# Optimization experiments

Hardware: AMD Instinct MI355X
Metric: run time of the kernel (lower is better)

Reference implementation:

```python
import jax, jax.numpy as jnp
import numpy as np
from jax import lax

M = 512      # num_centers
K = 32       # neighbors per center
FEAT = 256   # token feature dim
EPS = 1e-5   # BatchNorm eps


def fps(xyz, m):
    """Furthest point sampling. xyz: (B,N,3) -> idx (B,m) int32."""
    B, N, _ = xyz.shape
    first = jnp.zeros((B,), jnp.int32)

    def step(carry, _):
        min_d, last = carry                       # (B,N), (B,)
        last_pt = jnp.take_along_axis(xyz, last[:, None, None], axis=1)  # (B,1,3)
        d = jnp.sum((xyz - last_pt) ** 2, axis=-1)                       # (B,N)
        min_d = jnp.minimum(min_d, d)
        nxt = jnp.argmax(min_d, axis=1).astype(jnp.int32)
        return (min_d, nxt), nxt

    init = (jnp.full((B, N), 1e10, jnp.float32), first)
    _, rest = lax.scan(step, init, None, length=m - 1)   # (m-1, B)
    return jnp.concatenate([first[None, :], rest], axis=0).T  # (B,m)


def bn(x, g, b, mean, var):
    return (x - mean) * (g * lax.rsqrt(var + EPS)) + b


def setup_inputs() -> dict:
    key = jax.random.key(0)
    ks = jax.random.split(key, 16)
    B, N = 8, 16384
    r = lambda k_, s, sc=0.1: jax.random.normal(k_, s, jnp.float32) * sc
    inp = {
        "xyz": jax.random.normal(ks[0], (B, N, 3), jnp.float32),
        "W1": r(ks[1], (64, 3)), "b1": r(ks[2], (64,)),
        "g1": 1.0 + r(ks[3], (64,)), "be1": r(ks[4], (64,)),
        "m1": r(ks[5], (64,)), "v1": 1.0 + 0.1 * jax.random.uniform(ks[6], (64,)),
        "W2": r(ks[7], (128, 64)), "b2": r(ks[8], (128,)),
        "g2": 1.0 + r(ks[9], (128,)), "be2": r(ks[10], (128,)),
        "m2": r(ks[11], (128,)), "v2": 1.0 + 0.1 * jax.random.uniform(ks[12], (128,)),
        "W3": r(ks[13], (FEAT, 128)), "b3": r(ks[14], (FEAT,)),
        "Wp": r(ks[15], (FEAT, 3)), "bp": jnp.zeros((FEAT,), jnp.float32),
    }
    return inp


def reference(xyz, W1, b1, g1, be1, m1, v1, W2, b2, g2, be2, m2, v2, W3, b3, Wp, bp):
    B, N, _ = xyz.shape
    # --- FPS centers ---
    idx_c = fps(xyz, M)                                            # (B,M)
    centers = jnp.take_along_axis(xyz, idx_c[:, :, None], axis=1)  # (B,M,3)
    # --- brute-force KNN ---
    dist = jnp.sum((centers[:, :, None, :] - xyz[:, None, :, :]) ** 2, axis=-1)  # (B,M,N)
    _, idx = lax.top_k(-dist, K)                                   # (B,M,K)
    nbrs = jnp.take_along_axis(
        xyz, idx.reshape(B, M * K)[:, :, None], axis=1
    ).reshape(B, M, K, 3)
    grouped = nbrs - centers[:, :, None, :]                        # (B,M,K,3)
    # --- MiniPointNet: 1x1 convs == channel matmuls, eval-mode BN ---
    h = jnp.einsum("bmkc,oc->bmko", grouped, W1) + b1
    h = jax.nn.relu(bn(h, g1, be1, m1, v1))
    h = jnp.einsum("bmkc,oc->bmko", h, W2) + b2
    h = jax.nn.relu(bn(h, g2, be2, m2, v2))
    h = jnp.einsum("bmkc,oc->bmko", h, W3) + b3
    tokens = jnp.max(h, axis=2)                                    # (B,M,FEAT)
    pos = jnp.einsum("bmc,oc->bmo", centers, Wp) + bp
    return centers, tokens + pos
```

## Files before the change

### kernel.cpp

```cpp
#include <hip/hip_runtime.h>

typedef unsigned int u32;
typedef unsigned long long u64;
typedef unsigned short u16;

#define DEVFN static __device__ __forceinline__

constexpr int NPTS = 16384;
constexpr int NC = 512;

typedef __attribute__((ext_vector_type(8))) short bf16x8;
typedef __attribute__((ext_vector_type(4))) float f32x4;

#define MFMA16(a, b, c) __builtin_amdgcn_mfma_f32_16x16x32_bf16(a, b, c, 0, 0, 0)

DEVFN u16 bf16rne(float f) {
  u32 b = __float_as_uint(f);
  u32 r = (b + 0x7FFFu + ((b >> 16) & 1u)) >> 16;
  return (u16)r;
}

DEVFN u64 shflx64(u64 v, int m) {
  u32 lo = __shfl_xor((u32)v, m, 64);
  u32 hi = __shfl_xor((u32)(v >> 32), m, 64);
  return ((u64)hi << 32) | lo;
}
DEVFN u64 shfl64(u64 v, int src) {
  u32 lo = __shfl((u32)v, src, 64);
  u32 hi = __shfl((u32)(v >> 32), src, 64);
  return ((u64)hi << 32) | lo;
}

DEVFN void csw(u64& a, u64& b) {
  u64 lo = a < b ? a : b;
  u64 hi = a < b ? b : a;
  a = lo; b = hi;
}

DEVFN u32 spread3(u32 v) {
  return (v & 1u) | ((v & 2u) << 2) | ((v & 4u) << 4) | ((v & 8u) << 6);
}

DEVFN u64 maxf64u(u64 a, u64 b) {
  double x = __longlong_as_double((long long)a);
  double y = __longlong_as_double((long long)b);
  return (u64)__double_as_longlong(fmax(x, y));
}
template <int CTRL, int RM>
DEVFN u64 dppmaxf(u64 k) {
  u32 lo = (u32)k, hi = (u32)(k >> 32);
  u32 lo2 = (u32)__builtin_amdgcn_update_dpp((int)lo, (int)lo, CTRL, RM, 0xF, false);
  u32 hi2 = (u32)__builtin_amdgcn_update_dpp((int)hi, (int)hi, CTRL, RM, 0xF, false);
  return maxf64u(k, ((u64)hi2 << 32) | lo2);
}
DEVFN u64 wavemaxf(u64 k) {
  k = dppmaxf<0x121, 0xF>(k);
  k = dppmaxf<0x122, 0xF>(k);
  k = dppmaxf<0x124, 0xF>(k);
  k = dppmaxf<0x128, 0xF>(k);
  k = dppmaxf<0x142, 0xA>(k);
  k = dppmaxf<0x143, 0xC>(k);
  return k;
}

__global__ __launch_bounds__(1024) void fps_kernel(const float* __restrict__ xyz,
                                                   float* __restrict__ centers,
                                                   float4* __restrict__ ws4) {
  const int b = blockIdx.x;
  const int t = threadIdx.x;
  const int lane = t & 63;
  const int w = t >> 6;
  const float* xb = xyz + (size_t)b * NPTS * 3;
  const int bo = b * NPTS;

  __shared__ char smem[78336];
  float* mdL = (float*)smem;
  u64* ckeyL = (u64*)(smem + 65536);
  float* bboxT = (float*)(smem + 67584);
  float* ccoordL = (float*)(smem + 73728);
  u16* wl = (u16*)(smem + 76800);
  u32* wcnt = (u32*)(smem + 77824);
  float* redB = (float*)(smem + 77832);
  u32* redW = (u32*)(smem + 78248);
  u32* hist = (u32*)smem;
  u16* soidx = (u16*)(smem + 8192);

  const u32 inf10 = __float_as_uint(1e10f);

  u32 mcode[16];
  {
    float ox[16], oy[16], oz[16];
    float lx = 1e30f, ly = 1e30f, lz = 1e30f;
    float hx = -1e30f, hy = -1e30f, hz = -1e30f;
#pragma unroll
    for (int j = 0; j < 16; ++j) {
      int p = t + j * 1024;
      ox[j] = xb[p * 3 + 0];
      oy[j] = xb[p * 3 + 1];
      oz[j] = xb[p * 3 + 2];
      lx = fminf(lx, ox[j]); hx = fmaxf(hx, ox[j]);
      ly = fminf(ly, oy[j]); hy = fmaxf(hy, oy[j]);
      lz = fminf(lz, oz[j]); hz = fmaxf(hz, oz[j]);
    }
#pragma unroll
    for (int s = 32; s; s >>= 1) {
      lx = fminf(lx, __shfl_xor(lx, s, 64)); hx = fmaxf(hx, __shfl_xor(hx, s, 64));
      ly = fminf(ly, __shfl_xor(ly, s, 64)); hy = fmaxf(hy, __shfl_xor(hy, s, 64));
      lz = fminf(lz, __shfl_xor(lz, s, 64)); hz = fmaxf(hz, __shfl_xor(hz, s, 64));
    }
    if (lane == 0) {
      redB[w * 6 + 0] = lx; redB[w * 6 + 1] = hx;
      redB[w * 6 + 2] = ly; redB[w * 6 + 3] = hy;
      redB[w * 6 + 4] = lz; redB[w * 6 + 5] = hz;
    }
    hist[t] = 0; hist[t + 1024] = 0;
    if (t < 2) wcnt[t] = 0;
    __syncthreads();
    if (t == 0) {
      float a0 = redB[0], a1 = redB[1], a2 = redB[2], a3 = redB[3], a4 = redB[4], a5 = redB[5];
      for (int q = 1; q < 16; ++q) {
        a0 = fminf(a0, redB[q * 6 + 0]); a1 = fmaxf(a1, redB[q * 6 + 1]);
        a2 = fminf(a2, redB[q * 6 + 2]); a3 = fmaxf(a3, redB[q * 6 + 3]);
        a4 = fminf(a4, redB[q * 6 + 4]); a5 = fmaxf(a5, redB[q * 6 + 5]);
      }
      redB[96] = a0; redB[97] = a1; redB[98] = a2;
      redB[99] = a3; redB[100] = a4; redB[101] = a5;
    }
    __syncthreads();
    const float glx = redB[96], ghx = redB[97];
    const float gly = redB[98], ghy = redB[99];
    const float glz = redB[100], ghz = redB[101];
    const float sx = 15.999f / fmaxf(ghx - glx, 1e-9f);
    const float sy = 15.999f / fmaxf(ghy - gly, 1e-9f);
    const float sz = 7.999f / fmaxf(ghz - glz, 1e-9f);
#pragma unroll
    for (int j = 0; j < 16; ++j) {
      int ix = min(15, max(0, (int)((ox[j] - glx) * sx)));
      int iy = min(15, max(0, (int)((oy[j] - gly) * sy)));
      int iz = min(7, max(0, (int)((oz[j] - glz) * sz)));
      mcode[j] = spread3((u32)ix) | (spread3((u32)iy) << 1) | (spread3((u32)iz) << 2);
    }
  }
#pragma unroll
  for (int j = 0; j < 16; ++j) atomicAdd(&hist[mcode[j]], 1u);
  __syncthreads();
  {
    u32 h0 = hist[t * 2 + 0], h1 = hist[t * 2 + 1];
    u32 s = h0 + h1;
    u32 incl = s;
#pragma unroll
    for (int d = 1; d < 64; d <<= 1) {
      u32 n = __shfl_up(incl, d, 64);
      if (lane >= d) incl += n;
    }
    if (lane == 63) redW[w] = incl;
    __syncthreads();
    if (t == 0) {
      u32 run = 0;
      for (int q = 0; q < 16; ++q) { u32 tmp = redW[q]; redW[q] = run; run += tmp; }
    }
    __syncthreads();
    u32 exc = incl - s + redW[w];
    hist[t * 2 + 0] = exc;
    hist[t * 2 + 1] = exc + h0;
    __syncthreads();
  }
#pragma unroll
  for (int j = 0; j < 16; ++j) {
    u32 p = (u32)(t + j * 1024);
    u32 pos = atomicAdd(&hist[mcode[j]], 1u);
    soidx[pos] = (u16)p;
  }
  __syncthreads();
  {
    const int c = t >> 2;
    const int q = t & 3;
    float bxl = 1e30f, bxh = -1e30f, byl = 1e30f, byh = -1e30f, bzl = 1e30f, bzh = -1e30f;
    u32 lomax = 0;
    float axc = 0.f, ayc = 0.f, azc = 0.f;
#pragma unroll
    for (int j = 0; j < 16; ++j) {
      int sp = c * 64 + q * 16 + j;
      u32 oidx = (u32)soidx[sp];
      float X = xb[oidx * 3 + 0];
      float Y = xb[oidx * 3 + 1];
      float Z = xb[oidx * 3 + 2];
      u32 lo = ((16383u - oidx) << 8) | (u32)c;
      float4 pk; pk.x = X; pk.y = Y; pk.z = Z; pk.w = __uint_as_float(lo);
      ws4[bo + sp] = pk;
      if (lo > lomax) { lomax = lo; axc = X; ayc = Y; azc = Z; }
      bxl = fminf(bxl, X); bxh = fmaxf(bxh, X);
      byl = fminf(byl, Y); byh = fmaxf(byh, Y);
      bzl = fminf(bzl, Z); bzh = fmaxf(bzh, Z);
    }
    u32 gl = lomax;
#pragma unroll
    for (int s = 1; s <= 2; s <<= 1) {
      bxl = fminf(bxl, __shfl_xor(bxl, s, 64)); bxh = fmaxf(bxh, __shfl_xor(bxh, s, 64));
      byl = fminf(byl, __shfl_xor(byl, s, 64)); byh = fmaxf(byh, __shfl_xor(byh, s, 64));
      bzl = fminf(bzl, __shfl_xor(bzl, s, 64)); bzh = fmaxf(bzh, __shfl_xor(bzh, s, 64));
      gl = max(gl, (u32)__shfl_xor(gl, s, 64));
    }
    if (lomax == gl) {
      ccoordL[c * 3 + 0] = axc; ccoordL[c * 3 + 1] = ayc; ccoordL[c * 3 + 2] = azc;
    }
    if (q == 0) {
      bboxT[0 * 256 + c] = bxl; bboxT[1 * 256 + c] = bxh;
      bboxT[2 * 256 + c] = byl; bboxT[3 * 256 + c] = byh;
      bboxT[4 * 256 + c] = bzl; bboxT[5 * 256 + c] = bzh;
      ckeyL[c] = ((u64)inf10 << 32) | gl;
    }
  }
  __syncthreads();
#pragma unroll
  for (int j = 0; j < 16; ++j) mdL[t + j * 1024] = 1e10f;

  float cx = xb[0], cy = xb[1], cz = xb[2];
  if (t == 0) {
    centers[(b * NC) * 3 + 0] = cx;
    centers[(b * NC) * 3 + 1] = cy;
    centers[(b * NC) * 3 + 2] = cz;
  }

  for (int i = 1; i < NC; ++i) {
    if (t < 256) {
      float mdm = __uint_as_float((u32)(ckeyL[t] >> 32));
      float ax = fmaxf(0.f, fmaxf(__fsub_rn(bboxT[0 * 256 + t], cx), __fsub_rn(cx, bboxT[1 * 256 + t])));
      float ay = fmaxf(0.f, fmaxf(__fsub_rn(bboxT[2 * 256 + t], cy), __fsub_rn(cy, bboxT[3 * 256 + t])));
      float az = fmaxf(0.f, fmaxf(__fsub_rn(bboxT[4 * 256 + t], cz), __fsub_rn(cz, bboxT[5 * 256 + t])));
      float dlb = __fadd_rn(__fadd_rn(__fmul_rn(ax, ax), __fmul_rn(ay, ay)), __fmul_rn(az, az));
      if (dlb < mdm) {
        u32 pos = atomicAdd(&wcnt[i & 1], 1u);
        wl[(i & 1) * 256 + pos] = (u16)t;
      }
    } else if (t == 512) {
      wcnt[(i + 1) & 1] = 0u;
    }
    __syncthreads();
    {
      const int A = (int)wcnt[i & 1];
      for (int e = w; e < A; e += 16) {
        const int c = (int)wl[(i & 1) * 256 + e];
        const int sp = c * 64 + lane;
        float4 p = ws4[bo + sp];
        float dx = __fsub_rn(p.x, cx);
        float dy = __fsub_rn(p.y, cy);
        float dz = __fsub_rn(p.z, cz);
        float d = __fadd_rn(__fadd_rn(__fmul_rn(dx, dx), __fmul_rn(dy, dy)), __fmul_rn(dz, dz));
        float nm = fminf(mdL[sp], d);
        mdL[sp] = nm;
        u64 key = ((u64)__float_as_uint(nm) << 32) | (u64)__float_as_uint(p.w);
        u64 r = wavemaxf(key);
        u32 klo = (u32)__builtin_amdgcn_readlane((int)(u32)r, 63);
        u32 khi = (u32)__builtin_amdgcn_readlane((int)(u32)(r >> 32), 63);
        u64 wmax = ((u64)khi << 32) | klo;
        if (key == wmax) {
          ckeyL[c] = key;
          ccoordL[c * 3 + 0] = p.x; ccoordL[c * 3 + 1] = p.y; ccoordL[c * 3 + 2] = p.z;
        }
      }
    }
    __syncthreads();
    {
      u64 g0 = ckeyL[lane];
      u64 g1 = ckeyL[lane + 64];
      u64 g2 = ckeyL[lane + 128];
      u64 g3 = ckeyL[lane + 192];
      u64 g = maxf64u(maxf64u(g0, g1), maxf64u(g2, g3));
      g = wavemaxf(g);
      u32 glo = (u32)__builtin_amdgcn_readlane((int)(u32)g, 63);
      u32 widx = glo & 255u;
      cx = ccoordL[widx * 3 + 0];
      cy = ccoordL[widx * 3 + 1];
      cz = ccoordL[widx * 3 + 2];
      if (t == 0) {
        centers[(b * NC + i) * 3 + 0] = cx;
        centers[(b * NC + i) * 3 + 1] = cy;
        centers[(b * NC + i) * 3 + 2] = cz;
      }
    }
  }
}

__global__ __launch_bounds__(512) void knn_kernel(const float* __restrict__ xyz,
                                                  const float* __restrict__ centers,
                                                  float* __restrict__ grouped) {
  __shared__ float spts[1024 * 3];
  __shared__ u64 cand[8][192];
  __shared__ int ccnt[8];
  const int t = threadIdx.x;
  const int lane = t & 63;
  const int w = t >> 6;
  const int cg = blockIdx.x * 8 + w;
  const int b = cg >> 9;
  const float* xb = xyz + (size_t)b * NPTS * 3;
  const float cx = centers[cg * 3 + 0];
  const float cy = centers[cg * 3 + 1];
  const float cz = centers[cg * 3 + 2];
  if (lane == 0) ccnt[w] = 0;

  u64 lmin = ~0ull;
  for (int ch = 0; ch < 16; ++ch) {
    __syncthreads();
    const float* src = xb + ch * 1024 * 3;
#pragma unroll
    for (int q = 0; q < 6; ++q) spts[q * 512 + t] = src[q * 512 + t];
    __syncthreads();
#pragma unroll
    for (int j = 0; j < 16; ++j) {
      int p = lane + j * 64;
      float dx = __fsub_rn(cx, spts[p * 3 + 0]);
      float dy = __fsub_rn(cy, spts[p * 3 + 1]);
      float dz = __fsub_rn(cz, spts[p * 3 + 2]);
      float d = __fadd_rn(__fadd_rn(__fmul_rn(dx, dx), __fmul_rn(dy, dy)), __fmul_rn(dz, dz));
      u64 kk = ((u64)__float_as_uint(d) << 32) | (u64)(u32)(ch * 1024 + p);
      lmin = kk < lmin ? kk : lmin;
    }
  }
  u64 v = lmin;
  for (int k = 2; k <= 64; k <<= 1)
    for (int j = k >> 1; j > 0; j >>= 1) {
      u64 o = shflx64(v, j);
      bool up = ((lane & k) == 0);
      bool lowr = ((lane & j) == 0);
      u64 mn = v < o ? v : o;
      u64 mx = v < o ? o : v;
      v = (lowr == up) ? mn : mx;
    }
  u64 tau = shfl64(v, 31);
  float tf = __uint_as_float((u32)(tau >> 32));

  for (int ch = 0; ch < 16; ++ch) {
    __syncthreads();
    const float* src = xb + ch * 1024 * 3;
#pragma unroll
    for (int q = 0; q < 6; ++q) spts[q * 512 + t] = src[q * 512 + t];
    __syncthreads();
#pragma unroll
    for (int j = 0; j < 16; ++j) {
      int p = lane + j * 64;
      float dx = __fsub_rn(cx, spts[p * 3 + 0]);
      float dy = __fsub_rn(cy, spts[p * 3 + 1]);
      float dz = __fsub_rn(cz, spts[p * 3 + 2]);
      float d = __fadd_rn(__fadd_rn(__fmul_rn(dx, dx), __fmul_rn(dy, dy)), __fmul_rn(dz, dz));
      if (d <= tf) {
        int pos = atomicAdd(&ccnt[w], 1);
        if (pos < 192) cand[w][pos] = ((u64)__float_as_uint(d) << 32) | (u64)(u32)(ch * 1024 + p);
      }
    }
  }
  __syncthreads();
  int cnt = ccnt[w];
  u32 myn = 0u;
  if (cnt <= 192) {
    u64 c0 = (lane < cnt) ? cand[w][lane] : ~0ull;
    u64 c1 = (64 + lane < cnt) ? cand[w][64 + lane] : ~0ull;
    u64 c2 = (128 + lane < cnt) ? cand[w][128 + lane] : ~0ull;
    csw(c0, c1); csw(c1, c2); csw(c0, c1);
    for (int r = 0; r < 32; ++r) {
      u64 wm = c0;
      for (int s = 32; s; s >>= 1) {
        u64 o = shflx64(wm, s);
        wm = o < wm ? o : wm;
      }
      if (c0 == wm) { c0 = c1; c1 = c2; c2 = ~0ull; }
      if (lane == r) myn = (u32)wm;
    }
  } else {
    u64 last = 0ull;
    for (int r = 0; r < 32; ++r) {
      u64 bb = ~0ull;
      for (int j = 0; j < 256; ++j) {
        int p = lane + j * 64;
        float dx = __fsub_rn(cx, xb[p * 3 + 0]);
        float dy = __fsub_rn(cy, xb[p * 3 + 1]);
        float dz = __fsub_rn(cz, xb[p * 3 + 2]);
        float d = __fadd_rn(__fadd_rn(__fmul_rn(dx, dx), __fmul_rn(dy, dy)), __fmul_rn(dz, dz));
        u64 kk = ((u64)__float_as_uint(d) << 32) | (u64)(u32)p;
        if (r == 0 || kk > last)
          if (kk < bb) bb = kk;
      }
      for (int s = 32; s; s >>= 1) {
        u64 o = shflx64(bb, s);
        bb = o < bb ? o : bb;
      }
      last = bb;
      if (lane == r) myn = (u32)bb;
    }
  }
  if (lane < 32) {
    const float nx = xb[(size_t)myn * 3 + 0];
    const float ny = xb[(size_t)myn * 3 + 1];
    const float nz = xb[(size_t)myn * 3 + 2];
    float* gp = grouped + ((size_t)cg * 32 + lane) * 3;
    gp[0] = __fsub_rn(nx, cx);
    gp[1] = __fsub_rn(ny, cy);
    gp[2] = __fsub_rn(nz, cz);
  }
}

__global__ __launch_bounds__(256) void prep_kernel(
    const float* __restrict__ W1, const float* __restrict__ b1,
    const float* __restrict__ g1, const float* __restrict__ be1,
    const float* __restrict__ m1, const float* __restrict__ v1,
    const float* __restrict__ W2, const float* __restrict__ b2,
    const float* __restrict__ g2, const float* __restrict__ be2,
    const float* __restrict__ m2, const float* __restrict__ v2,
    const float* __restrict__ W3,
    float* __restrict__ w1eff, u16* __restrict__ w2L,
    float* __restrict__ t2, u16* __restrict__ w3L) {
  const int tid = blockIdx.x * 256 + threadIdx.x;
  if (tid < 64) {
    float s = g1[tid] / sqrtf(v1[tid] + 1e-5f);
    w1eff[tid * 4 + 0] = W1[tid * 3 + 0] * s;
    w1eff[tid * 4 + 1] = W1[tid * 3 + 1] * s;
    w1eff[tid * 4 + 2] = W1[tid * 3 + 2] * s;
    w1eff[tid * 4 + 3] = (b1[tid] - m1[tid]) * s + be1[tid];
  }
  if (tid < 128) {
    float s = g2[tid] / sqrtf(v2[tid] + 1e-5f);
    t2[tid] = (b2[tid] - m2[tid]) * s + be2[tid];
  }
  if (tid < 8192) {
    int i = tid & 63, o = tid >> 6;
    float s = g2[o] / sqrtf(v2[o] + 1e-5f);
    int kg = i >> 3, j = i & 7;
    w2L[((((kg * 128) + o) * 8) ^ ((kg & 7) * 8)) + j] = bf16rne(W2[o * 64 + i] * s);
  }
  if (tid < 32768) {
    int i = tid & 127, o = tid >> 7;
    int kg = i >> 3, j = i & 7;
    int h = o >> 7, colh = o & 127;
    w3L[h * 16384 + ((((kg * 128) + colh) * 8) ^ ((kg & 7) * 8)) + j] = bf16rne(W3[o * 128 + i]);
  }
}

__global__ __launch_bounds__(256) void mlp_kernel(
    const float* __restrict__ grouped, const u16* __restrict__ w2L,
    const u16* __restrict__ w3L, const float* __restrict__ w1eff,
    const float* __restrict__ t2, const float* __restrict__ b3,
    const float* __restrict__ Wp, const float* __restrict__ bp,
    const float* __restrict__ centers, float* __restrict__ tokens) {
  __shared__ char lds[65536];
  const int t = threadIdx.x;
  const int lane = t & 63;
  const int w = t >> 6;
  const int l15 = lane & 15;
  const int lg = lane >> 4;
  const int c0 = blockIdx.x * 4;
  {
    const u32* s = (const u32*)w2L;
    u32* d = (u32*)lds;
#pragma unroll
    for (int q = 0; q < 16; ++q) d[q * 256 + t] = s[q * 256 + t];
  }
  {
    const int row = t & 127;
    const int oh = (t >> 7) * 32;
    const int cg = c0 + (row >> 5);
    const float* gp = grouped + ((size_t)cg * 32 + (row & 31)) * 3;
    const float gx = gp[0], gy = gp[1], gz = gp[2];
    u16 hv[32];
#pragma unroll
    for (int o = 0; o < 32; ++o) {
      const float4 wvv = ((const float4*)w1eff)[oh + o];
      float h = fmaxf(0.f, gx * wvv.x + gy * wvv.y + gz * wvv.z + wvv.w);
      hv[o] = bf16rne(h);
    }
#pragma unroll
    for (int c4 = 0; c4 < 4; ++c4) {
      uint4 pk;
      pk.x = (u32)hv[c4 * 8 + 0] | ((u32)hv[c4 * 8 + 1] << 16);
      pk.y = (u32)hv[c4 * 8 + 2] | ((u32)hv[c4 * 8 + 3] << 16);
      pk.z = (u32)hv[c4 * 8 + 4] | ((u32)hv[c4 * 8 + 5] << 16);
      pk.w = (u32)hv[c4 * 8 + 6] | ((u32)hv[c4 * 8 + 7] << 16);
      int byte = row * 128 + oh * 2 + c4 * 16;
      *reinterpret_cast<uint4*>(lds + 16384 + (byte ^ ((row & 7) << 4))) = pk;
    }
  }
  __syncthreads();
  f32x4 acc2[2][8];
#pragma unroll
  for (int m = 0; m < 2; ++m)
#pragma unroll
    for (int n = 0; n < 8; ++n) acc2[m][n] = (f32x4){0.f, 0.f, 0.f, 0.f};
#pragma unroll
  for (int ks = 0; ks < 2; ++ks) {
    bf16x8 a[2];
#pragma unroll
    for (int m = 0; m < 2; ++m) {
      int row = w * 32 + m * 16 + l15;
      int byte = row * 128 + (ks * 32 + lg * 8) * 2;
      a[m] = *reinterpret_cast<const bf16x8*>(lds + 16384 + (byte ^ ((row & 7) << 4)));
    }
    const int kg = ks * 4 + lg;
#pragma unroll
    for (int n = 0; n < 8; ++n) {
      int idx = (((kg * 128) + (n * 16 + l15)) * 8) ^ ((kg & 7) * 8);
      bf16x8 bb = *reinterpret_cast<const bf16x8*>((const u16*)lds + idx);
      acc2[0][n] = MFMA16(a[0], bb, acc2[0][n]);
      acc2[1][n] = MFMA16(a[1], bb, acc2[1][n]);
    }
  }
#pragma unroll
  for (int n = 0; n < 8; ++n) {
    const int col = n * 16 + l15;
    const float t2v = t2[col];
#pragma unroll
    for (int m = 0; m < 2; ++m)
#pragma unroll
      for (int r = 0; r < 4; ++r) {
        float vv = fmaxf(0.f, acc2[m][n][r] + t2v);
        int row = w * 32 + m * 16 + lg * 4 + r;
        int byte = row * 256 + col * 2;
        *reinterpret_cast<u16*>(lds + 32768 + (byte ^ ((row & 7) << 4))) = bf16rne(vv);
      }
  }
  __syncthreads();
  const float ccx = centers[(c0 + w) * 3 + 0];
  const float ccy = centers[(c0 + w) * 3 + 1];
  const float ccz = centers[(c0 + w) * 3 + 2];
  float* tok = tokens + (size_t)(c0 + w) * 256;
  for (int h = 0; h < 2; ++h) {
    {
      const u32* s = (const u32*)w3L + h * 8192;
      u32* d = (u32*)lds;
#pragma unroll
      for (int q = 0; q < 32; ++q) d[q * 256 + t] = s[q * 256 + t];
    }
    __syncthreads();
    f32x4 acc3[2][8];
#pragma unroll
    for (int m = 0; m < 2; ++m)
#pragma unroll
      for (int n = 0; n < 8; ++n) acc3[m][n] = (f32x4){0.f, 0.f, 0.f, 0.f};
#pragma unroll
    for (int ks = 0; ks < 4; ++ks) {
      bf16x8 a[2];
#pragma unroll
      for (int m = 0; m < 2; ++m) {
        int row = w * 32 + m * 16 + l15;
        int byte = row * 256 + (ks * 32 + lg * 8) * 2;
        a[m] = *reinterpret_cast<const bf16x8*>(lds + 32768 + (byte ^ ((row & 7) << 4)));
      }
      const int kg = ks * 4 + lg;
#pragma unroll
      for (int n = 0; n < 8; ++n) {
        int idx = (((kg * 128) + (n * 16 + l15)) * 8) ^ ((kg & 7) * 8);
        bf16x8 bb = *reinterpret_cast<const bf16x8*>((const u16*)lds + idx);
        acc3[0][n] = MFMA16(a[0], bb, acc3[0][n]);
        acc3[1][n] = MFMA16(a[1], bb, acc3[1][n]);
      }
    }
#pragma unroll
    for (int n = 0; n < 8; ++n) {
      float vmx = acc3[0][n][0];
#pragma unroll
      for (int m = 0; m < 2; ++m)
#pragma unroll
        for (int r = 0; r < 4; ++r) vmx = fmaxf(vmx, acc3[m][n][r]);
      vmx = fmaxf(vmx, __shfl_xor(vmx, 16, 64));
      vmx = fmaxf(vmx, __shfl_xor(vmx, 32, 64));
      const int col = h * 128 + n * 16 + l15;
      if (lane < 16) {
        float pos = Wp[col * 3 + 0] * ccx + Wp[col * 3 + 1] * ccy +
                    Wp[col * 3 + 2] * ccz + bp[col] + b3[col];
        tok[col] = vmx + pos;
      }
    }
    __syncthreads();
  }
}

extern "C" void kernel_launch(void* const* d_in, const int* in_sizes, int n_in,
                              void* d_out, int out_size, void* d_ws, size_t ws_size,
                              hipStream_t stream) {
  const float* xyz = (const float*)d_in[0];
  const float* W1 = (const float*)d_in[1];
  const float* b1 = (const float*)d_in[2];
  const float* g1 = (const float*)d_in[3];
  const float* be1 = (const float*)d_in[4];
  const float* m1 = (const float*)d_in[5];
  const float* v1 = (const float*)d_in[6];
  const float* W2 = (const float*)d_in[7];
  const float* b2 = (const float*)d_in[8];
  const float* g2 = (const float*)d_in[9];
  const float* be2 = (const float*)d_in[10];
  const float* m2 = (const float*)d_in[11];
  const float* v2 = (const float*)d_in[12];
  const float* W3 = (const float*)d_in[13];
  const float* b3 = (const float*)d_in[14];
  const float* Wp = (const float*)d_in[15];
  const float* bp = (const float*)d_in[16];

  char* ws = (char*)d_ws;
  float4* ws4 = (float4*)ws;
  float* grouped = (float*)ws;
  float* w1eff = (float*)(ws + 2097152);
  u16* w2L = (u16*)(ws + 2098176);
  float* t2 = (float*)(ws + 2114560);
  u16* w3L = (u16*)(ws + 2115072);

  float* centers = (float*)d_out;
  float* tokens = (float*)d_out + 8 * 512 * 3;

  prep_kernel<<<dim3(128), dim3(256), 0, stream>>>(W1, b1, g1, be1, m1, v1,
                                                   W2, b2, g2, be2, m2, v2, W3,
                                                   w1eff, w2L, t2, w3L);
  fps_kernel<<<dim3(8), dim3(1024), 0, stream>>>(xyz, centers, ws4);
  knn_kernel<<<dim3(512), dim3(512), 0, stream>>>(xyz, centers, grouped);
  mlp_kernel<<<dim3(1024), dim3(256), 0, stream>>>(grouped, w2L, w3L, w1eff, t2,
                                                   b3, Wp, bp, centers, tokens);
}
```

Baseline: 832.6 us.

## Move FPS argmax into bbox-test waves and broadcast center via LDS

The per-iteration global argmax over cell keys used to run on all 16 waves. It now runs only in the four waves that do the bounding-box culling, at the start of the next iteration, and the winner is broadcast to the other waves through a small LDS slot. The worklist append switches from one LDS atomic per active thread to one atomic per wave, using a ballot and mbcnt. The wave-max match compares only the low 32 bits, saving one readlane. The goal is less redundant work and fewer atomics on the serial FPS critical path, at the cost of an extra LDS read per iteration and a final argmax after the loop.

```diff
diff --git a/kernel.cpp b/kernel.cpp
--- a/kernel.cpp
+++ b/kernel.cpp
@@ -73,7 +73,7 @@
   const float* xb = xyz + (size_t)b * NPTS * 3;
   const int bo = b * NPTS;
 
-  __shared__ char smem[78336];
+  __shared__ char smem[78352];
   float* mdL = (float*)smem;
   u64* ckeyL = (u64*)(smem + 65536);
   float* bboxT = (float*)(smem + 67584);
@@ -82,6 +82,7 @@
   u32* wcnt = (u32*)(smem + 77824);
   float* redB = (float*)(smem + 77832);
   u32* redW = (u32*)(smem + 78248);
+  float* cxyzL = (float*)(smem + 78336);
   u32* hist = (u32*)smem;
   u16* soidx = (u16*)(smem + 8192);
 
@@ -220,27 +221,54 @@
     centers[(b * NC) * 3 + 0] = cx;
     centers[(b * NC) * 3 + 1] = cy;
     centers[(b * NC) * 3 + 2] = cz;
+    cxyzL[0] = cx; cxyzL[1] = cy; cxyzL[2] = cz;
   }
 
   for (int i = 1; i < NC; ++i) {
     if (t < 256) {
+      if (i > 1) {
+        u64 g0 = ckeyL[lane];
+        u64 g1 = ckeyL[lane + 64];
+        u64 g2 = ckeyL[lane + 128];
+        u64 g3 = ckeyL[lane + 192];
+        u64 g = maxf64u(maxf64u(g0, g1), maxf64u(g2, g3));
+        g = wavemaxf(g);
+        u32 glo = (u32)__builtin_amdgcn_readlane((int)(u32)g, 63);
+        u32 widx = glo & 255u;
+        cx = ccoordL[widx * 3 + 0];
+        cy = ccoordL[widx * 3 + 1];
+        cz = ccoordL[widx * 3 + 2];
+        if (t == 0) {
+          centers[(b * NC + i - 1) * 3 + 0] = cx;
+          centers[(b * NC + i - 1) * 3 + 1] = cy;
+          centers[(b * NC + i - 1) * 3 + 2] = cz;
+          cxyzL[0] = cx; cxyzL[1] = cy; cxyzL[2] = cz;
+        }
+      }
       float mdm = __uint_as_float((u32)(ckeyL[t] >> 32));
       float ax = fmaxf(0.f, fmaxf(__fsub_rn(bboxT[0 * 256 + t], cx), __fsub_rn(cx, bboxT[1 * 256 + t])));
       float ay = fmaxf(0.f, fmaxf(__fsub_rn(bboxT[2 * 256 + t], cy), __fsub_rn(cy, bboxT[3 * 256 + t])));
       float az = fmaxf(0.f, fmaxf(__fsub_rn(bboxT[4 * 256 + t], cz), __fsub_rn(cz, bboxT[5 * 256 + t])));
       float dlb = __fadd_rn(__fadd_rn(__fmul_rn(ax, ax), __fmul_rn(ay, ay)), __fmul_rn(az, az));
-      if (dlb < mdm) {
-        u32 pos = atomicAdd(&wcnt[i & 1], 1u);
-        wl[(i & 1) * 256 + pos] = (u16)t;
-      }
-    } else if (t == 512) {
+      bool act = dlb < mdm;
+      u64 bal = __ballot(act);
+      u32 cnt = (u32)__popcll(bal);
+      u32 base = 0;
+      if (lane == 0) base = atomicAdd(&wcnt[i & 1], cnt);
+      base = (u32)__builtin_amdgcn_readlane((int)base, 0);
+      u32 below = __builtin_amdgcn_mbcnt_hi((u32)(bal >> 32),
+                  __builtin_amdgcn_mbcnt_lo((u32)bal, 0));
+      if (act) wl[(i & 1) * 256 + base + below] = (u16)t;
+    } else if (t == 256) {
       wcnt[(i + 1) & 1] = 0u;
     }
     __syncthreads();
     {
+      cx = cxyzL[0]; cy = cxyzL[1]; cz = cxyzL[2];
       const int A = (int)wcnt[i & 1];
+      const u16* wlp = wl + (i & 1) * 256;
       for (int e = w; e < A; e += 16) {
-        const int c = (int)wl[(i & 1) * 256 + e];
+        const int c = (int)wlp[e];
         const int sp = c * 64 + lane;
         float4 p = ws4[bo + sp];
         float dx = __fsub_rn(p.x, cx);
@@ -251,33 +279,28 @@
         mdL[sp] = nm;
         u64 key = ((u64)__float_as_uint(nm) << 32) | (u64)__float_as_uint(p.w);
         u64 r = wavemaxf(key);
-        u32 klo = (u32)__builtin_amdgcn_readlane((int)(u32)r, 63);
-        u32 khi = (u32)__builtin_amdgcn_readlane((int)(u32)(r >> 32), 63);
-        u64 wmax = ((u64)khi << 32) | klo;
-        if (key == wmax) {
+        u32 rlo = (u32)__builtin_amdgcn_readlane((int)(u32)r, 63);
+        if ((u32)key == rlo) {
           ckeyL[c] = key;
           ccoordL[c * 3 + 0] = p.x; ccoordL[c * 3 + 1] = p.y; ccoordL[c * 3 + 2] = p.z;
         }
       }
     }
     __syncthreads();
-    {
-      u64 g0 = ckeyL[lane];
-      u64 g1 = ckeyL[lane + 64];
-      u64 g2 = ckeyL[lane + 128];
-      u64 g3 = ckeyL[lane + 192];
-      u64 g = maxf64u(maxf64u(g0, g1), maxf64u(g2, g3));
-      g = wavemaxf(g);
-      u32 glo = (u32)__builtin_amdgcn_readlane((int)(u32)g, 63);
-      u32 widx = glo & 255u;
-      cx = ccoordL[widx * 3 + 0];
-      cy = ccoordL[widx * 3 + 1];
-      cz = ccoordL[widx * 3 + 2];
-      if (t == 0) {
-        centers[(b * NC + i) * 3 + 0] = cx;
-        centers[(b * NC + i) * 3 + 1] = cy;
-        centers[(b * NC + i) * 3 + 2] = cz;
-      }
+  }
+  if (w == 0) {
+    u64 g0 = ckeyL[lane];
+    u64 g1 = ckeyL[lane + 64];
+    u64 g2 = ckeyL[lane + 128];
+    u64 g3 = ckeyL[lane + 192];
+    u64 g = maxf64u(maxf64u(g0, g1), maxf64u(g2, g3));
+    g = wavemaxf(g);
+    u32 glo = (u32)__builtin_amdgcn_readlane((int)(u32)g, 63);
+    u32 widx = glo & 255u;
+    if (t == 0) {
+      centers[(b * NC + NC - 1) * 3 + 0] = ccoordL[widx * 3 + 0];
+      centers[(b * NC + NC - 1) * 3 + 1] = ccoordL[widx * 3 + 1];
+      centers[(b * NC + NC - 1) * 3 + 2] = ccoordL[widx * 3 + 2];
     }
   }
 }
```

New measurement: 827.1 us. Within noise of the previous version (-0.7%).

## Restructure FPS loop: static cell-to-wave ownership, one barrier per iteration

Applied to the files above, without the earlier changes.

Each wave now statically owns 16 of the 256 spatial cells and keeps their bounding boxes and best keys in registers. The shared atomic worklist is replaced by a ballot mask over the wave's cells. Each wave publishes its local best key and coordinates into a double-buffered shared slot, and every wave reduces the 16 slots at the start of the next iteration. This removes two of the three block barriers per FPS step and the atomics. The cost is possible load imbalance when active cells cluster on a few waves, plus redundant per-wave reductions.

```diff
diff --git a/kernel.cpp b/kernel.cpp
--- a/kernel.cpp
+++ b/kernel.cpp
@@ -73,15 +73,14 @@
   const float* xb = xyz + (size_t)b * NPTS * 3;
   const int bo = b * NPTS;
 
-  __shared__ char smem[78336];
+  __shared__ char smem[78080];
   float* mdL = (float*)smem;
-  u64* ckeyL = (u64*)(smem + 65536);
-  float* bboxT = (float*)(smem + 67584);
-  float* ccoordL = (float*)(smem + 73728);
-  u16* wl = (u16*)(smem + 76800);
-  u32* wcnt = (u32*)(smem + 77824);
-  float* redB = (float*)(smem + 77832);
-  u32* redW = (u32*)(smem + 78248);
+  float* ccoordL = (float*)(smem + 65536);
+  u32* swb = (u32*)(smem + 68608);
+  u64* ckeyL = (u64*)(smem + 69376);
+  float* bboxT = (float*)(smem + 71424);
+  float* redB = (float*)(smem + 77568);
+  u32* redW = (u32*)(smem + 77984);
   u32* hist = (u32*)smem;
   u16* soidx = (u16*)(smem + 8192);
 
@@ -114,7 +113,6 @@
       redB[w * 6 + 4] = lz; redB[w * 6 + 5] = hz;
     }
     hist[t] = 0; hist[t + 1024] = 0;
-    if (t < 2) wcnt[t] = 0;
     __syncthreads();
     if (t == 0) {
       float a0 = redB[0], a1 = redB[1], a2 = redB[2], a3 = redB[3], a4 = redB[4], a5 = redB[5];
@@ -214,70 +212,118 @@
   __syncthreads();
 #pragma unroll
   for (int j = 0; j < 16; ++j) mdL[t + j * 1024] = 1e10f;
-
-  float cx = xb[0], cy = xb[1], cz = xb[2];
+  u64 ckeyR = 0ull;
+  float rbxl = 0.f, rbxh = 0.f, rbyl = 0.f, rbyh = 0.f, rbzl = 0.f, rbzh = 0.f;
+  if (lane < 16) {
+    const int c = (lane << 4) | w;
+    ckeyR = ckeyL[c];
+    rbxl = bboxT[0 * 256 + c]; rbxh = bboxT[1 * 256 + c];
+    rbyl = bboxT[2 * 256 + c]; rbyh = bboxT[3 * 256 + c];
+    rbzl = bboxT[4 * 256 + c]; rbzh = bboxT[5 * 256 + c];
+  }
+  {
+    u64 v = (lane < 16) ? ckeyR : 0ull;
+    v = wavemaxf(v);
+    u32 vlo = (u32)__builtin_amdgcn_readlane((int)(u32)v, 63);
+    u32 vhi = (u32)__builtin_amdgcn_readlane((int)(u32)(v >> 32), 63);
+    if (lane == 0) {
+      u32 sc = vlo & 255u;
+      u32* dst = swb + 0 * 96 + w * 6;
+      dst[0] = vhi; dst[1] = vlo;
+      dst[2] = __float_as_uint(ccoordL[sc * 3 + 0]);
+      dst[3] = __float_as_uint(ccoordL[sc * 3 + 1]);
+      dst[4] = __float_as_uint(ccoordL[sc * 3 + 2]);
+    }
+  }
   if (t == 0) {
-    centers[(b * NC) * 3 + 0] = cx;
-    centers[(b * NC) * 3 + 1] = cy;
-    centers[(b * NC) * 3 + 2] = cz;
-  }
+    centers[(b * NC) * 3 + 0] = xb[0];
+    centers[(b * NC) * 3 + 1] = xb[1];
+    centers[(b * NC) * 3 + 2] = xb[2];
+  }
+  __syncthreads();
 
   for (int i = 1; i < NC; ++i) {
-    if (t < 256) {
-      float mdm = __uint_as_float((u32)(ckeyL[t] >> 32));
-      float ax = fmaxf(0.f, fmaxf(__fsub_rn(bboxT[0 * 256 + t], cx), __fsub_rn(cx, bboxT[1 * 256 + t])));
-      float ay = fmaxf(0.f, fmaxf(__fsub_rn(bboxT[2 * 256 + t], cy), __fsub_rn(cy, bboxT[3 * 256 + t])));
-      float az = fmaxf(0.f, fmaxf(__fsub_rn(bboxT[4 * 256 + t], cz), __fsub_rn(cz, bboxT[5 * 256 + t])));
+    const u32* sw = swb + ((i - 1) & 1) * 96;
+    const int row = lane & 15;
+    u32 khi = sw[row * 6 + 0];
+    u32 klo = sw[row * 6 + 1];
+    u64 g = ((u64)khi << 32) | klo;
+    u64 gm = wavemaxf(g);
+    u32 glo = (u32)__builtin_amdgcn_readlane((int)(u32)gm, 63);
+    u32 ghi = (u32)__builtin_amdgcn_readlane((int)(u32)(gm >> 32), 63);
+    bool win = (lane < 16) && (klo == glo) && (khi == ghi);
+    u64 bal = __ballot(win);
+    int wrow = (int)(__ffsll((unsigned long long)bal) - 1);
+    float cx = __uint_as_float(sw[wrow * 6 + 2]);
+    float cy = __uint_as_float(sw[wrow * 6 + 3]);
+    float cz = __uint_as_float(sw[wrow * 6 + 4]);
+    if (t == 0) {
+      centers[(b * NC + i - 1) * 3 + 0] = cx;
+      centers[(b * NC + i - 1) * 3 + 1] = cy;
+      centers[(b * NC + i - 1) * 3 + 2] = cz;
+    }
+    bool act = false;
+    if (lane < 16) {
+      float mdm = __uint_as_float((u32)(ckeyR >> 32));
+      float ax = fmaxf(0.f, fmaxf(__fsub_rn(rbxl, cx), __fsub_rn(cx, rbxh)));
+      float ay = fmaxf(0.f, fmaxf(__fsub_rn(rbyl, cy), __fsub_rn(cy, rbyh)));
+      float az = fmaxf(0.f, fmaxf(__fsub_rn(rbzl, cz), __fsub_rn(cz, rbzh)));
       float dlb = __fadd_rn(__fadd_rn(__fmul_rn(ax, ax), __fmul_rn(ay, ay)), __fmul_rn(az, az));
-      if (dlb < mdm) {
-        u32 pos = atomicAdd(&wcnt[i & 1], 1u);
-        wl[(i & 1) * 256 + pos] = (u16)t;
-      }
-    } else if (t == 512) {
-      wcnt[(i + 1) & 1] = 0u;
-    }
-    __syncthreads();
-    {
-      const int A = (int)wcnt[i & 1];
-      for (int e = w; e < A; e += 16) {
-        const int c = (int)wl[(i & 1) * 256 + e];
-        const int sp = c * 64 + lane;
-        float4 p = ws4[bo + sp];
-        float dx = __fsub_rn(p.x, cx);
-        float dy = __fsub_rn(p.y, cy);
-        float dz = __fsub_rn(p.z, cz);
-        float d = __fadd_rn(__fadd_rn(__fmul_rn(dx, dx), __fmul_rn(dy, dy)), __fmul_rn(dz, dz));
-        float nm = fminf(mdL[sp], d);
-        mdL[sp] = nm;
-        u64 key = ((u64)__float_as_uint(nm) << 32) | (u64)__float_as_uint(p.w);
-        u64 r = wavemaxf(key);
-        u32 klo = (u32)__builtin_amdgcn_readlane((int)(u32)r, 63);
-        u32 khi = (u32)__builtin_amdgcn_readlane((int)(u32)(r >> 32), 63);
-        u64 wmax = ((u64)khi << 32) | klo;
-        if (key == wmax) {
-          ckeyL[c] = key;
-          ccoordL[c * 3 + 0] = p.x; ccoordL[c * 3 + 1] = p.y; ccoordL[c * 3 + 2] = p.z;
-        }
-      }
-    }
-    __syncthreads();
-    {
-      u64 g0 = ckeyL[lane];
-      u64 g1 = ckeyL[lane + 64];
-      u64 g2 = ckeyL[lane + 128];
-      u64 g3 = ckeyL[lane + 192];
-      u64 g = maxf64u(maxf64u(g0, g1), maxf64u(g2, g3));
-      g = wavemaxf(g);
-      u32 glo = (u32)__builtin_amdgcn_readlane((int)(u32)g, 63);
-      u32 widx = glo & 255u;
-      cx = ccoordL[widx * 3 + 0];
-      cy = ccoordL[widx * 3 + 1];
-      cz = ccoordL[widx * 3 + 2];
-      if (t == 0) {
-        centers[(b * NC + i) * 3 + 0] = cx;
-        centers[(b * NC + i) * 3 + 1] = cy;
-        centers[(b * NC + i) * 3 + 2] = cz;
-      }
+      act = dlb < mdm;
+    }
+    u32 mask = (u32)__ballot(act) & 0xFFFFu;
+    while (mask) {
+      const int s = __ffs(mask) - 1;
+      mask &= mask - 1;
+      const int c = (s << 4) | w;
+      const int sp = c * 64 + lane;
+      float4 p = ws4[bo + sp];
+      float dx = __fsub_rn(p.x, cx);
+      float dy = __fsub_rn(p.y, cy);
+      float dz = __fsub_rn(p.z, cz);
+      float d = __fadd_rn(__fadd_rn(__fmul_rn(dx, dx), __fmul_rn(dy, dy)), __fmul_rn(dz, dz));
+      float nm = fminf(mdL[sp], d);
+      mdL[sp] = nm;
+      u64 key = ((u64)__float_as_uint(nm) << 32) | (u64)__float_as_uint(p.w);
+      u64 r = wavemaxf(key);
+      u32 rlo = (u32)__builtin_amdgcn_readlane((int)(u32)r, 63);
+      u32 rhi = (u32)__builtin_amdgcn_readlane((int)(u32)(r >> 32), 63);
+      u64 wmax = ((u64)rhi << 32) | rlo;
+      if ((u32)key == rlo) {
+        ccoordL[c * 3 + 0] = p.x; ccoordL[c * 3 + 1] = p.y; ccoordL[c * 3 + 2] = p.z;
+      }
+      if (lane == s) ckeyR = wmax;
+    }
+    u64 v = (lane < 16) ? ckeyR : 0ull;
+    v = wavemaxf(v);
+    u32 vlo = (u32)__builtin_amdgcn_readlane((int)(u32)v, 63);
+    u32 vhi = (u32)__builtin_amdgcn_readlane((int)(u32)(v >> 32), 63);
+    if (lane == 0) {
+      u32 sc = vlo & 255u;
+      u32* dst = swb + (i & 1) * 96 + w * 6;
+      dst[0] = vhi; dst[1] = vlo;
+      dst[2] = __float_as_uint(ccoordL[sc * 3 + 0]);
+      dst[3] = __float_as_uint(ccoordL[sc * 3 + 1]);
+      dst[4] = __float_as_uint(ccoordL[sc * 3 + 2]);
+    }
+    __syncthreads();
+  }
+  {
+    const u32* sw = swb + ((NC - 1) & 1) * 96;
+    const int row = lane & 15;
+    u32 khi = sw[row * 6 + 0];
+    u32 klo = sw[row * 6 + 1];
+    u64 g = ((u64)khi << 32) | klo;
+    u64 gm = wavemaxf(g);
+    u32 glo = (u32)__builtin_amdgcn_readlane((int)(u32)gm, 63);
+    u32 ghi = (u32)__builtin_amdgcn_readlane((int)(u32)(gm >> 32), 63);
+    bool win = (lane < 16) && (klo == glo) && (khi == ghi);
+    u64 bal = __ballot(win);
+    int wrow = (int)(__ffsll((unsigned long long)bal) - 1);
+    if (t == 0) {
+      centers[(b * NC + NC - 1) * 3 + 0] = __uint_as_float(sw[wrow * 6 + 2]);
+      centers[(b * NC + NC - 1) * 3 + 1] = __uint_as_float(sw[wrow * 6 + 3]);
+      centers[(b * NC + NC - 1) * 3 + 2] = __uint_as_float(sw[wrow * 6 + 4]);
     }
   }
 }
```

Result: slower. 1.023 ms (+22.9%).
